# Kernel tuning notes

Measured on AMD Instinct MI355X. Metric: run time of the kernel, lower is better.

## Reference

```python
import jax, jax.numpy as jnp
import numpy as np

H = 2048          # hidden_size
L_CACHE = 3       # depthwise conv kernel size
BATCH, SEQ = 2, 4096


def setup_inputs() -> dict:
    key = jax.random.key(0)
    k1, k2, k3, k4 = jax.random.split(key, 4)
    hidden_states = jax.random.normal(k1, (BATCH, SEQ, H), dtype=jnp.float32)
    # torch nn.Linear weights: [out_features, in_features]
    W_in = jax.random.normal(k2, (3 * H, H), dtype=jnp.float32) * (1.0 / np.sqrt(H))
    W_out = jax.random.normal(k3, (H, H), dtype=jnp.float32) * (1.0 / np.sqrt(H))
    # torch depthwise Conv1d weight: [H, 1, L]
    W_conv = jax.random.normal(k4, (H, 1, L_CACHE), dtype=jnp.float32) * (1.0 / np.sqrt(L_CACHE))
    return {"hidden_states": hidden_states, "W_in": W_in, "W_conv": W_conv, "W_out": W_out}


def reference(hidden_states, W_in, W_conv, W_out):
    # in_proj: [B,S,H] @ [H,3H] -> [B,S,3H]
    BCx = jnp.einsum('bsh,oh->bso', hidden_states, W_in)
    Bg, Cg, x = jnp.split(BCx, 3, axis=-1)   # each [B,S,H]
    Bx = Bg * x                              # gate before conv
    # depthwise causal conv over sequence: operate in NCH layout
    Bx_nch = jnp.transpose(Bx, (0, 2, 1))    # [B,H,S]
    conv_out = jax.lax.conv_general_dilated(
        Bx_nch, W_conv,
        window_strides=(1,),
        padding=[(L_CACHE - 1, 0)],          # causal: left pad only
        dimension_numbers=('NCH', 'OIH', 'NCH'),
        feature_group_count=H,
    )                                        # [B,H,S]
    y = Cg * jnp.transpose(conv_out, (0, 2, 1))  # C gating, back to [B,S,H]
    return jnp.einsum('bsh,oh->bso', y, W_out)   # out_proj
```

## Files before the change

### kernel.cpp

```cpp
#include <hip/hip_runtime.h>
#include <hip/hip_fp16.h>


typedef _Float16 f16x8 __attribute__((ext_vector_type(8)));
typedef float    f32x4 __attribute__((ext_vector_type(4)));

#define GLD_LDS16(gsrc, sdst) \
  __builtin_amdgcn_global_load_lds((const __attribute__((address_space(1))) void*)(gsrc), \
                                   (__attribute__((address_space(3))) void*)(sdst), 16, 0, 0)

#define VMCNT4 asm volatile("s_waitcnt vmcnt(4)" ::: "memory")
#define VMCNT0 asm volatile("s_waitcnt vmcnt(0)" ::: "memory")
#define LGKM0  asm volatile("s_waitcnt lgkmcnt(0)" ::: "memory")
#define BAR    __builtin_amdgcn_s_barrier()
#define SCHED0 __builtin_amdgcn_sched_barrier(0)

__global__ __launch_bounds__(256) void cvt_f32_f16(const float* __restrict__ in,
                                                   _Float16* __restrict__ out, int n) {
  int i = blockIdx.x * 256 + threadIdx.x;
  int base = i * 8;
  if (base >= n) return;
  const float4* p = reinterpret_cast<const float4*>(in) + i * 2;
  float4 a = p[0], b = p[1];
  f16x8 o;
  o[0] = (_Float16)a.x; o[1] = (_Float16)a.y; o[2] = (_Float16)a.z; o[3] = (_Float16)a.w;
  o[4] = (_Float16)b.x; o[5] = (_Float16)b.y; o[6] = (_Float16)b.z; o[7] = (_Float16)b.w;
  *reinterpret_cast<f16x8*>(out + base) = o;
}

__global__ __launch_bounds__(256) void conv_gate(const _Float16* __restrict__ BCx,
                                                 const float* __restrict__ Wc,
                                                 _Float16* __restrict__ Y) {
  const int h0 = threadIdx.x * 8;
  const int r0 = blockIdx.x * 8;
  const int s0 = r0 & 4095;

  float w0[8], w1[8], w2[8];
#pragma unroll
  for (int j = 0; j < 8; ++j) {
    w0[j] = Wc[(h0 + j) * 3 + 0];
    w1[j] = Wc[(h0 + j) * 3 + 1];
    w2[j] = Wc[(h0 + j) * 3 + 2];
  }

  float bxm2[8] = {}, bxm1[8] = {};
  if (s0 != 0) {
    const _Float16* pm2 = BCx + (size_t)(r0 - 2) * 6144 + h0;
    const _Float16* pm1 = BCx + (size_t)(r0 - 1) * 6144 + h0;
    f16x8 bg2 = *reinterpret_cast<const f16x8*>(pm2);
    f16x8 xx2 = *reinterpret_cast<const f16x8*>(pm2 + 4096);
    f16x8 bg1 = *reinterpret_cast<const f16x8*>(pm1);
    f16x8 xx1 = *reinterpret_cast<const f16x8*>(pm1 + 4096);
#pragma unroll
    for (int j = 0; j < 8; ++j) {
      bxm2[j] = (float)bg2[j] * (float)xx2[j];
      bxm1[j] = (float)bg1[j] * (float)xx1[j];
    }
  }

  for (int i = 0; i < 8; ++i) {
    const _Float16* pr = BCx + (size_t)(r0 + i) * 6144 + h0;
    f16x8 bg = *reinterpret_cast<const f16x8*>(pr);
    f16x8 cg = *reinterpret_cast<const f16x8*>(pr + 2048);
    f16x8 xx = *reinterpret_cast<const f16x8*>(pr + 4096);
    f16x8 o;
#pragma unroll
    for (int j = 0; j < 8; ++j) {
      float bx   = (float)bg[j] * (float)xx[j];
      float conv = w0[j] * bxm2[j] + w1[j] * bxm1[j] + w2[j] * bx;
      o[j] = (_Float16)((float)cg[j] * conv);
      bxm2[j] = bxm1[j];
      bxm1[j] = bx;
    }
    *reinterpret_cast<f16x8*>(Y + (size_t)(r0 + i) * 2048 + h0) = o;
  }
}

__device__ __forceinline__ void ldA(f16x8 (&af)[4][2], const _Float16* p, int base, int ak0, int ak1) {
#pragma unroll
  for (int i = 0; i < 4; ++i) {
    af[i][0] = *(const f16x8*)(p + base + i * 1024 + ak0);
    af[i][1] = *(const f16x8*)(p + base + i * 1024 + ak1);
  }
}
__device__ __forceinline__ void ldB(f16x8 (&bf)[2][2], const _Float16* p, int base, int ak0, int ak1) {
#pragma unroll
  for (int j = 0; j < 2; ++j) {
    bf[j][0] = *(const f16x8*)(p + base + j * 1024 + ak0);
    bf[j][1] = *(const f16x8*)(p + base + j * 1024 + ak1);
  }
}
template <int QM, int QN>
__device__ __forceinline__ void mfmaQ(f32x4 (&acc)[8][4], const f16x8 (&af)[4][2], const f16x8 (&bf)[2][2]) {
  __builtin_amdgcn_s_setprio(1);
#pragma unroll
  for (int i = 0; i < 4; ++i)
#pragma unroll
    for (int j = 0; j < 2; ++j)
#pragma unroll
      for (int ks = 0; ks < 2; ++ks)
        acc[QM * 4 + i][QN * 2 + j] =
            __builtin_amdgcn_mfma_f32_16x16x32_f16(af[i][ks], bf[j][ks], acc[QM * 4 + i][QN * 2 + j], 0, 0, 0);
  __builtin_amdgcn_s_setprio(0);
}

template <typename CT>
__global__ __launch_bounds__(512, 2) void gemm8p(const _Float16* __restrict__ Ag,
                                                 const _Float16* __restrict__ Bg,
                                                 CT* __restrict__ Cg,
                                                 int N, int K, int nbn) {
  __shared__ __align__(16) char smem[131072];
  const int tid = threadIdx.x, lane = tid & 63, w = tid >> 6;
  const int wr = w >> 2, wc = w & 3;

  const int nwg = (int)gridDim.x, q8 = nwg >> 3;
  const int swz = ((int)blockIdx.x & 7) * q8 + ((int)blockIdx.x >> 3);
  const int bm = (swz / nbn) << 8, bn = (swz % nbn) << 8;

  _Float16* const A0 = (_Float16*)(smem);
  _Float16* const B0 = (_Float16*)(smem + 32768);
  _Float16* const A1 = (_Float16*)(smem + 65536);
  _Float16* const B1 = (_Float16*)(smem + 98304);

  const int rr = tid >> 3;
  const int sCol = ((tid & 7) ^ (rr & 7)) * 8;
  const _Float16* aSrc = Ag + (size_t)(bm + rr) * K + sCol;
  const _Float16* bSrc = Bg + (size_t)(bn + (rr >> 5) * 64 + (rr & 31)) * K + sCol;

  const int ak0 = ((lane >> 4) ^ (lane & 7)) * 8;
  const int ak1 = (((lane >> 4) + 4) ^ (lane & 7)) * 8;
  const int aRB = (wr * 128 + (lane & 15)) * 64;
  const int bRB = (wc * 32 + (lane & 15)) * 64;

  const int nt = K >> 6;

#define STG_A(NBO, kt, u) GLD_LDS16(aSrc + (size_t)(u) * 64 * K + (kt) * 64, \
                                    smem + (NBO) + (u) * 8192 + tid * 16)
#define STG_B(NBO, kt, u) GLD_LDS16(bSrc + (size_t)(((u) & 1) * 128 + ((u) >> 1) * 32) * K + (kt) * 64, \
                                    smem + (NBO) + 32768 + (u) * 8192 + tid * 16)

  f16x8 af[4][2], bf[2][2];
  f32x4 acc[8][4] = {};

  STG_A(0, 0, 0); STG_A(0, 0, 2);
  STG_B(0, 0, 0); STG_B(0, 0, 1);
  STG_B(0, 0, 2); STG_B(0, 0, 3);
  STG_A(0, 0, 1); STG_A(0, 0, 3);
  VMCNT4; BAR;

#define TILE(AB, BB, NBO, t)                                       \
  {                                                                \
    const int tn = ((t) + 1 < nt) ? (t) + 1 : nt - 1;              \
                                                  \
    ldA(af, AB, aRB, ak0, ak1);                                    \
    ldB(bf, BB, bRB, ak0, ak1);                                    \
    STG_A(NBO, tn, 0); STG_A(NBO, tn, 2);                          \
    VMCNT4; BAR; LGKM0; SCHED0;                                    \
    mfmaQ<0, 0>(acc, af, bf);                                      \
                                                  \
    ldB(bf, BB, bRB + 8192, ak0, ak1);                             \
    STG_B(NBO, tn, 0); STG_B(NBO, tn, 1);                          \
    VMCNT4; BAR; LGKM0; SCHED0;                                    \
    mfmaQ<0, 1>(acc, af, bf);                                      \
                                                  \
    ldA(af, AB, aRB + 4096, ak0, ak1);                             \
    STG_B(NBO, tn, 2); STG_B(NBO, tn, 3);                          \
    BAR; LGKM0; SCHED0;                                            \
    mfmaQ<1, 1>(acc, af, bf);                                      \
                                \
    ldB(bf, BB, bRB, ak0, ak1);                                    \
    STG_A(NBO, tn, 1); STG_A(NBO, tn, 3);                          \
    VMCNT4; BAR; LGKM0; SCHED0;                                    \
    mfmaQ<1, 0>(acc, af, bf);                                      \
  }

  for (int t = 0; t < nt; t += 2) {
    TILE(A0, B0, 65536, t);
    TILE(A1, B1, 0, t + 1);
  }
  VMCNT0;

  const int rb = bm + wr * 128 + ((lane >> 4) << 2);
  const int cb = bn + wc * 64 + (lane & 15);
#pragma unroll
  for (int mi = 0; mi < 8; ++mi)
#pragma unroll
    for (int nj = 0; nj < 4; ++nj) {
      f32x4 v = acc[mi][nj];
#pragma unroll
      for (int rg = 0; rg < 4; ++rg)
        Cg[(size_t)(rb + mi * 16 + rg) * N + cb + nj * 16] = (CT)v[rg];
    }
#undef TILE
#undef STG_A
#undef STG_B
}

extern "C" void kernel_launch(void* const* d_in, const int* in_sizes, int n_in,
                              void* d_out, int out_size, void* d_ws, size_t ws_size,
                              hipStream_t stream) {
  const float* X  = (const float*)d_in[0];
  const float* Wi = (const float*)d_in[1];
  const float* Wc = (const float*)d_in[2];
  const float* Wo = (const float*)d_in[3];
  float* out = (float*)d_out;

  char* ws = (char*)d_ws;
  _Float16* Xh   = (_Float16*)(ws);
  _Float16* Wih  = (_Float16*)(ws + 33554432);
  _Float16* Woh  = (_Float16*)(ws + 58720256);
  _Float16* BCxh = (_Float16*)(ws + 67108864);
  _Float16* Yh   = (_Float16*)(ws + 167772160);
  (void)ws_size; (void)in_sizes; (void)n_in; (void)out_size;

  cvt_f32_f16<<<dim3(16777216 / 2048), 256, 0, stream>>>(X,  Xh,  16777216);
  cvt_f32_f16<<<dim3(12582912 / 2048), 256, 0, stream>>>(Wi, Wih, 12582912);
  cvt_f32_f16<<<dim3( 4194304 / 2048), 256, 0, stream>>>(Wo, Woh,  4194304);

  gemm8p<_Float16><<<dim3(768), 512, 0, stream>>>(Xh, Wih, BCxh, 6144, 2048, 24);

  conv_gate<<<dim3(1024), 256, 0, stream>>>(BCxh, Wc, Yh);

  gemm8p<float><<<dim3(256), 512, 0, stream>>>(Yh, Woh, out, 2048, 2048, 8);
}
```

Before: 302.1 us.

## Software-pipeline LDS fragment loads one quarter ahead of MFMA in GEMM loop

Restructures the GEMM main loop so each quarter issues the LDS reads for the next quarter's A/B fragments before running the current quarter's MFMAs. It uses separate register sets for A halves and for three rotating B fragments, and prefetches the next tile's first fragments across the tile boundary. Wait counts tighten to vmcnt(2), and the prologue now waits for all loads. The aim is to hide LDS read latency behind matrix math, at the cost of more VGPRs, which may lower occupancy or cause spills, and a subtler barrier/buffer-reuse ordering.

New measurement: 306.3 us. Within noise of the previous version (+1.4%).

```diff
diff --git a/kernel.cpp b/kernel.cpp
--- a/kernel.cpp
+++ b/kernel.cpp
@@ -9,7 +9,7 @@
   __builtin_amdgcn_global_load_lds((const __attribute__((address_space(1))) void*)(gsrc), \
                                    (__attribute__((address_space(3))) void*)(sdst), 16, 0, 0)
 
-#define VMCNT4 asm volatile("s_waitcnt vmcnt(4)" ::: "memory")
+#define VMCNT2 asm volatile("s_waitcnt vmcnt(2)" ::: "memory")
 #define VMCNT0 asm volatile("s_waitcnt vmcnt(0)" ::: "memory")
 #define LGKM0  asm volatile("s_waitcnt lgkmcnt(0)" ::: "memory")
 #define BAR    __builtin_amdgcn_s_barrier()
@@ -139,44 +139,50 @@
 #define STG_B(NBO, kt, u) GLD_LDS16(bSrc + (size_t)(((u) & 1) * 128 + ((u) >> 1) * 32) * K + (kt) * 64, \
                                     smem + (NBO) + 32768 + (u) * 8192 + tid * 16)
 
-  f16x8 af[4][2], bf[2][2];
+  f16x8 afL[4][2], afH[4][2];
+  f16x8 bfA[2][2], bfB[2][2], bfC[2][2];
   f32x4 acc[8][4] = {};
 
   STG_A(0, 0, 0); STG_A(0, 0, 2);
   STG_B(0, 0, 0); STG_B(0, 0, 1);
   STG_B(0, 0, 2); STG_B(0, 0, 3);
   STG_A(0, 0, 1); STG_A(0, 0, 3);
-  VMCNT4; BAR;
-
-#define TILE(AB, BB, NBO, t)                                       \
+  VMCNT0; BAR;
+  ldA(afL, A0, aRB, ak0, ak1);
+  ldB(bfA, B0, bRB, ak0, ak1);
+
+#define TILE(AB, BB, ABn, BBn, NBO, t, BF0, BF0N)                  \
   {                                                                \
     const int tn = ((t) + 1 < nt) ? (t) + 1 : nt - 1;              \
-                                                  \
-    ldA(af, AB, aRB, ak0, ak1);                                    \
-    ldB(bf, BB, bRB, ak0, ak1);                                    \
+                                \
+    LGKM0; SCHED0;                                                 \
+    ldB(bfB, BB, bRB + 8192, ak0, ak1);                            \
+    mfmaQ<0, 0>(acc, afL, BF0);                                    \
     STG_A(NBO, tn, 0); STG_A(NBO, tn, 2);                          \
-    VMCNT4; BAR; LGKM0; SCHED0;                                    \
-    mfmaQ<0, 0>(acc, af, bf);                                      \
-                                                  \
-    ldB(bf, BB, bRB + 8192, ak0, ak1);                             \
+    VMCNT2; BAR;                                                   \
+                                \
+    LGKM0; SCHED0;                                                 \
+    ldA(afH, AB, aRB + 4096, ak0, ak1);                            \
+    mfmaQ<0, 1>(acc, afL, bfB);                                    \
     STG_B(NBO, tn, 0); STG_B(NBO, tn, 1);                          \
-    VMCNT4; BAR; LGKM0; SCHED0;                                    \
-    mfmaQ<0, 1>(acc, af, bf);                                      \
-                                                  \
-    ldA(af, AB, aRB + 4096, ak0, ak1);                             \
+    VMCNT2; BAR;                                                   \
+             \
+    LGKM0; SCHED0;                                                 \
+    ldA(afL, ABn, aRB, ak0, ak1);                                  \
+    mfmaQ<1, 1>(acc, afH, bfB);                                    \
     STG_B(NBO, tn, 2); STG_B(NBO, tn, 3);                          \
-    BAR; LGKM0; SCHED0;                                            \
-    mfmaQ<1, 1>(acc, af, bf);                                      \
-                                \
-    ldB(bf, BB, bRB, ak0, ak1);                                    \
+    VMCNT2; BAR;                                                   \
+             \
+    LGKM0; SCHED0;                                                 \
+    ldB(BF0N, BBn, bRB, ak0, ak1);                                 \
+    mfmaQ<1, 0>(acc, afH, BF0);                                    \
     STG_A(NBO, tn, 1); STG_A(NBO, tn, 3);                          \
-    VMCNT4; BAR; LGKM0; SCHED0;                                    \
-    mfmaQ<1, 0>(acc, af, bf);                                      \
+    VMCNT2; BAR;                                                   \
   }
 
   for (int t = 0; t < nt; t += 2) {
-    TILE(A0, B0, 65536, t);
-    TILE(A1, B1, 0, t + 1);
+    TILE(A0, B0, A1, B1, 65536, t,     bfA, bfC);
+    TILE(A1, B1, A0, B0, 0,     t + 1, bfC, bfA);
   }
   VMCNT0;
 
```
